# Kernel optimization log

Measured on AMD Instinct MI355X. Metric: run time of the kernel, lower is better.

Reference implementation:

```python
import jax, jax.numpy as jnp
import numpy as np

TREE_DEPTH = 3
CONSTANTS = jnp.array([-1.0, 0.0, 1.0], dtype=jnp.float32)


def setup_inputs() -> dict:
    key = jax.random.key(0)
    ks = jax.random.split(key, 5)
    B, S, D, W, SLOT = 2, 2048, 1024, 4096, 8
    C = SLOT + 3
    hidden = jax.random.normal(ks[0], (B, S, D), dtype=jnp.float32)
    slot_w = jax.random.normal(ks[1], (D, SLOT), dtype=jnp.float32) * (0.5 / np.sqrt(D))
    slot_b = jnp.zeros((SLOT,), dtype=jnp.float32)
    leaf_logits = jax.random.normal(ks[2], (W, 1 << TREE_DEPTH, C), dtype=jnp.float32) * 0.02
    node_params = jnp.array([1.0, 1.0, 0.25, 0.0, 0.0], dtype=jnp.float32)
    out_w = jax.random.normal(ks[3], (W, D), dtype=jnp.float32) * (0.5 / np.sqrt(W))
    out_b = jnp.zeros((D,), dtype=jnp.float32)
    return {"hidden": hidden, "slot_w": slot_w, "slot_b": slot_b,
            "leaf_logits": leaf_logits, "node_params": node_params,
            "out_w": out_w, "out_b": out_b}


def reference(hidden, slot_w, slot_b, leaf_logits, node_params, out_w, out_b):
    B, S, _ = hidden.shape
    # basis: tanh slot projection concatenated with fixed constants -> [B,S,slot+3]
    slots = jnp.tanh(hidden @ slot_w + slot_b)
    consts = jnp.broadcast_to(CONSTANTS.astype(hidden.dtype), (B, S, 3))
    basis = jnp.concatenate((slots, consts), axis=-1)
    # leaf values: softmax-weighted mixture over the tiny basis dim -> [B,S,W,leaf]
    selector = jax.nn.softmax(leaf_logits.astype(hidden.dtype), axis=-1)
    values = jnp.einsum('wlc,bsc->bswl', selector, basis)
    lw, rw, pw, dw, nb = [p.astype(hidden.dtype) for p in node_params]
    for _ in range(TREE_DEPTH):
        left, right = values[..., 0::2], values[..., 1::2]
        values = jnp.tanh(lw * left + rw * right + pw * left * right
                          + dw * (left - right) + nb)
    roots = values[..., 0]  # [B,S,W]
    return roots @ out_w + out_b
```

## Files before the change

kernel.cpp:

```cpp
#include <hip/hip_runtime.h>
#include <stdint.h>

#define BSZ   4096
#define DIM   1024
#define WTR   4096
#define KDIM  4096
#define W8    32768

typedef unsigned short u16;
typedef __attribute__((ext_vector_type(8))) short bhalf8;
typedef __attribute__((ext_vector_type(4))) float floatx4;
typedef __attribute__((ext_vector_type(16))) float floatx16;

__device__ __forceinline__ u16 f2bf(float f) {
    union { float f; uint32_t i; } v; v.f = f;
    uint32_t r = v.i + 0x7fffu + ((v.i >> 16) & 1u);
    return (u16)(r >> 16);
}
__device__ __forceinline__ float fast_tanh(float x) {
    float e = __builtin_amdgcn_exp2f(x * 2.885390081777927f);
    return fmaf(-2.0f, __builtin_amdgcn_rcpf(e + 1.0f), 1.0f);
}
__device__ __forceinline__ void load16(const void* g, void* lds) {
    __builtin_amdgcn_global_load_lds(
        (const __attribute__((address_space(1))) uint32_t*)g,
        (__attribute__((address_space(3))) uint32_t*)lds, 16, 0, 0);
}

__global__ __launch_bounds__(256) void k_prep(const float* __restrict__ ll,
                                              u16* __restrict__ selwA,
                                              const float* __restrict__ ow,
                                              u16* __restrict__ owt,
                                              const float* __restrict__ slot_w,
                                              u16* __restrict__ swT,
                                              const float* __restrict__ out_b,
                                              float* __restrict__ C) {
    int bid = blockIdx.x, tid = threadIdx.x;
    if (bid < 128) {
        int row = bid * 256 + tid;
        int w = row >> 3, l = row & 7, q = w & 3;
        int prow = (w >> 2) * 32 + (l & 3) + 8 * (l >> 2) + 16 * (q & 1) + 4 * (q >> 1);
        const float* p = ll + (size_t)row * 11;
        float v[11]; float m = -1e30f;
        #pragma unroll
        for (int c = 0; c < 11; ++c) { v[c] = p[c]; m = fmaxf(m, v[c]); }
        float s = 0.f;
        #pragma unroll
        for (int c = 0; c < 11; ++c) {
            v[c] = __builtin_amdgcn_exp2f((v[c] - m) * 1.4426950408889634f);
            s += v[c];
        }
        float inv = __builtin_amdgcn_rcpf(s);
        union { u16 h[16]; uint4 qq[2]; } o;
        #pragma unroll
        for (int c = 0; c < 8; ++c) o.h[c] = f2bf(v[c] * inv);
        o.h[8] = f2bf((v[10] - v[8]) * inv);
        #pragma unroll
        for (int c = 9; c < 16; ++c) o.h[c] = 0;
        uint4* dst = (uint4*)(selwA + (size_t)prow * 16);
        dst[0] = o.qq[0]; dst[1] = o.qq[1];
    } else if (bid < 128 + 4096) {
        int b = bid - 128;
        int d0 = (b & 31) * 32, w0 = (b >> 5) * 32;
        int tx = tid & 31, ty = tid >> 5;
        __shared__ float tile[32][33];
        #pragma unroll
        for (int i = 0; i < 32; i += 8)
            tile[ty + i][tx] = ow[(size_t)(w0 + ty + i) * DIM + d0 + tx];
        __syncthreads();
        #pragma unroll
        for (int i = 0; i < 32; i += 8)
            owt[(size_t)(d0 + ty + i) * WTR + w0 + tx] = f2bf(tile[tx][ty + i]);
    } else if (bid < 128 + 4096 + 8) {
        int b = bid - 128 - 4096;
        for (int it = 0; it < 8; ++it) {
            int idx = b * 2048 + it * 256 + tid;
            int s = idx >> 10, d = idx & 1023;
            float val = (s < 8) ? slot_w[(size_t)d * 8 + s] : 0.f;
            swT[(size_t)s * DIM + d] = f2bf(val);
        }
    } else {
        int b = bid - 128 - 4096 - 8;
        float4 bv = *(const float4*)(out_b + (tid & 255) * 4);
        #pragma unroll
        for (int it = 0; it < 16; ++it) {
            size_t flat = (size_t)b * 16384 + it * 1024 + (tid & 255) * 4;
            *(float4*)(C + flat) = bv;
        }
    }
}

__global__ __launch_bounds__(256) void k_basis(const float* __restrict__ hidden,
                                               const u16* __restrict__ swT,
                                               const float* __restrict__ slot_b,
                                               u16* __restrict__ basisTB) {
    int m0 = blockIdx.x * 16;
    int tid = threadIdx.x, lane = tid & 63, wid = tid >> 6;
    int col = lane & 15, quad = lane >> 4;
    const float* ga = hidden + (size_t)(m0 + col) * DIM + wid * 256 + quad * 8;
    const u16*   gb = swT + (size_t)col * DIM + wid * 256 + quad * 8;
    floatx4 acc = (floatx4){0.f, 0.f, 0.f, 0.f};
    #pragma unroll
    for (int k0 = 0; k0 < 256; k0 += 32) {
        float4 a0 = *(const float4*)(ga + k0);
        float4 a1 = *(const float4*)(ga + k0 + 4);
        bhalf8 bf = *(const bhalf8*)(gb + k0);
        bhalf8 af;
        af[0] = (short)f2bf(a0.x); af[1] = (short)f2bf(a0.y);
        af[2] = (short)f2bf(a0.z); af[3] = (short)f2bf(a0.w);
        af[4] = (short)f2bf(a1.x); af[5] = (short)f2bf(a1.y);
        af[6] = (short)f2bf(a1.z); af[7] = (short)f2bf(a1.w);
        acc = __builtin_amdgcn_mfma_f32_16x16x32_bf16(af, bf, acc, 0, 0, 0);
    }
    __shared__ float smr[4][16][16];
    #pragma unroll
    for (int r = 0; r < 4; ++r) smr[wid][quad * 4 + r][col] = acc[r];
    __syncthreads();
    int tt = tid >> 4, cc = tid & 15;
    float s = smr[0][tt][cc] + smr[1][tt][cc] + smr[2][tt][cc] + smr[3][tt][cc];
    u16 val;
    if (cc < 8)       val = f2bf(fast_tanh(s + slot_b[cc]));
    else if (cc == 8) val = (u16)0x3f80;
    else              val = 0;
    basisTB[(size_t)(m0 + tt) * 16 + cc] = val;
}

__device__ __forceinline__ float tree_eval(float v[8], float A1, float A2,
                                           float A3, float A4) {
    #pragma unroll
    for (int lev = 0; lev < 3; ++lev) {
        int n = 4 >> lev;
        #pragma unroll
        for (int i = 0; i < 4; ++i) {
            if (i < n) {
                float L = v[2*i], R = v[2*i+1];
                float u = fmaf(A2, R, A1);
                float w = fmaf(A3, R, A4);
                float y = fmaf(L, u, w);
                float e = __builtin_amdgcn_exp2f(y);
                v[i] = fmaf(-2.0f, __builtin_amdgcn_rcpf(e + 1.0f), 1.0f);
            }
        }
    }
    return v[0];
}

__global__ __launch_bounds__(256, 2) void k_roots(const u16* __restrict__ selwA,
                                                  const u16* __restrict__ basisTB,
                                                  const float* __restrict__ np_,
                                                  u16* __restrict__ roots) {
    __shared__ uint32_t st[2][32 * 33];
    int tid = threadIdx.x, wid = tid >> 6, lane = tid & 63;
    int c = lane & 31, h = lane >> 5;
    int tile0 = blockIdx.x * 16 + wid * 4;
    int wblk  = blockIdx.x * 64;
    int t0b   = blockIdx.y * 512;
    float lw = np_[0], rw = np_[1], pw = np_[2], dw = np_[3], nb = np_[4];
    const float c2 = 2.885390081777927f;
    float A1 = (lw + dw) * c2, A2 = pw * c2, A3 = (rw - dw) * c2, A4 = nb * c2;

    bhalf8 af[4];
    #pragma unroll
    for (int tl = 0; tl < 4; ++tl)
        af[tl] = *(const bhalf8*)(selwA + (size_t)((tile0 + tl) * 32 + c) * 16 + h * 8);

    int tok = tid >> 3, ch = tid & 7;
    for (int it = 0; it < 16; ++it) {
        int t0 = t0b + it * 32;
        uint32_t* buf = st[it & 1];
        bhalf8 bf = *(const bhalf8*)(basisTB + (size_t)(t0 + c) * 16 + h * 8);
        #pragma unroll
        for (int tl = 0; tl < 4; ++tl) {
            floatx16 z = {0.f,0.f,0.f,0.f,0.f,0.f,0.f,0.f,
                          0.f,0.f,0.f,0.f,0.f,0.f,0.f,0.f};
            floatx16 cc = __builtin_amdgcn_mfma_f32_32x32x16_bf16(af[tl], bf, z, 0, 0, 0);
            float vA[8], vB[8];
            #pragma unroll
            for (int l = 0; l < 8; ++l) { vA[l] = cc[l]; vB[l] = cc[8 + l]; }
            float rA = tree_eval(vA, A1, A2, A3, A4);
            float rB = tree_eval(vB, A1, A2, A3, A4);
            buf[c * 33 + wid * 8 + tl * 2 + h] =
                (uint32_t)f2bf(rA) | ((uint32_t)f2bf(rB) << 16);
        }
        __syncthreads();
        uint32_t d0 = buf[tok * 33 + ch * 4];
        uint32_t d1 = buf[tok * 33 + ch * 4 + 1];
        uint32_t d2 = buf[tok * 33 + ch * 4 + 2];
        uint32_t d3 = buf[tok * 33 + ch * 4 + 3];
        uint4 q; q.x = d0; q.y = d1; q.z = d2; q.w = d3;
        *(uint4*)(roots + (size_t)(t0 + tok) * WTR + wblk + ch * 8) = q;
    }
}

__global__ __launch_bounds__(256) void k_gemm(const u16* __restrict__ A,
                                              const u16* __restrict__ Bt,
                                              float* __restrict__ C) {
    __shared__ __align__(16) u16 smA[128 * 64];
    __shared__ __align__(16) u16 smB[128 * 64];
    int tid = threadIdx.x;
    int bm = blockIdx.x * 128, bn = blockIdx.y * 128;
    int koff = blockIdx.z * (KDIM / 2);
    int lane = tid & 63, wid = tid >> 6;
    int wm = (wid >> 1) * 64, wn = (wid & 1) * 64;

    floatx4 acc[4][4];
    #pragma unroll
    for (int i = 0; i < 4; ++i)
        #pragma unroll
        for (int j = 0; j < 4; ++j) acc[i][j] = (floatx4){0.f, 0.f, 0.f, 0.f};

    int ar = tid >> 3;
    int ak = ((tid & 7) ^ (ar & 7)) * 8;
    const u16* gA = A  + (size_t)(bm + ar) * KDIM + koff + ak;
    const u16* gB = Bt + (size_t)(bn + ar) * KDIM + koff + ak;
    char* ldA = (char*)smA + tid * 16;
    char* ldB = (char*)smB + tid * 16;

    int col = lane & 15, quad = lane >> 4, csw = col & 7;

    for (int k0 = 0; k0 < KDIM / 2 / 64; ++k0) {
        __syncthreads();
        load16(gA,                       ldA);
        load16(gA + (size_t)32 * KDIM,   ldA + 4096);
        load16(gA + (size_t)64 * KDIM,   ldA + 8192);
        load16(gA + (size_t)96 * KDIM,   ldA + 12288);
        load16(gB,                       ldB);
        load16(gB + (size_t)32 * KDIM,   ldB + 4096);
        load16(gB + (size_t)64 * KDIM,   ldB + 8192);
        load16(gB + (size_t)96 * KDIM,   ldB + 12288);
        gA += 64; gB += 64;
        __syncthreads();

        #pragma unroll
        for (int kk = 0; kk < 2; ++kk) {
            int kc = kk * 4 + quad;
            bhalf8 af[4], bf[4];
            #pragma unroll
            for (int i = 0; i < 4; ++i)
                af[i] = *(const bhalf8*)(smA + ((wm + i * 16 + col) * 8 + (kc ^ csw)) * 8);
            #pragma unroll
            for (int j = 0; j < 4; ++j)
                bf[j] = *(const bhalf8*)(smB + ((wn + j * 16 + col) * 8 + (kc ^ csw)) * 8);
            #pragma unroll
            for (int i = 0; i < 4; ++i)
                #pragma unroll
                for (int j = 0; j < 4; ++j)
                    acc[i][j] = __builtin_amdgcn_mfma_f32_16x16x32_bf16(
                        af[i], bf[j], acc[i][j], 0, 0, 0);
        }
    }

    #pragma unroll
    for (int j = 0; j < 4; ++j) {
        int n = bn + wn + j * 16 + col;
        #pragma unroll
        for (int i = 0; i < 4; ++i) {
            int m0 = bm + wm + i * 16 + quad * 4;
            #pragma unroll
            for (int r = 0; r < 4; ++r)
                atomicAdd(&C[(size_t)(m0 + r) * DIM + n], acc[i][j][r]);
        }
    }
}

extern "C" void kernel_launch(void* const* d_in, const int* in_sizes, int n_in,
                              void* d_out, int out_size, void* d_ws, size_t ws_size,
                              hipStream_t stream) {
    const float* hidden      = (const float*)d_in[0];
    const float* slot_w      = (const float*)d_in[1];
    const float* slot_b      = (const float*)d_in[2];
    const float* leaf_logits = (const float*)d_in[3];
    const float* node_params = (const float*)d_in[4];
    const float* out_w       = (const float*)d_in[5];
    const float* out_b       = (const float*)d_in[6];
    float* out = (float*)d_out;

    char* ws = (char*)d_ws;
    u16* selwA   = (u16*)ws;
    u16* basisTB = (u16*)(ws + 1048576);
    u16* swT     = (u16*)(ws + 1179648);
    u16* outwt   = (u16*)(ws + 1212416);
    u16* roots   = (u16*)(ws + 9601024);

    k_prep <<<128 + 4096 + 8 + 256, 256, 0, stream>>>(leaf_logits, selwA, out_w, outwt,
                                                      slot_w, swT, out_b, out);
    k_basis<<<BSZ / 16, 256, 0, stream>>>(hidden, swT, slot_b, basisTB);
    k_roots<<<dim3(64, 8), 256, 0, stream>>>(selwA, basisTB, node_params, roots);
    k_gemm <<<dim3(BSZ / 128, DIM / 128, 2), 256, 0, stream>>>(roots, outwt, out);
}
```

Measured before the change: 190.8 us.

## Fold basis projection into prep kernel and split GEMM K four ways

The separate basis-projection kernel is merged into the prep kernel as extra blocks. Each of those blocks transposes slot_w into shared memory itself, so the swT workspace buffer and one kernel launch go away. The output GEMM now splits K four ways instead of two, with a 32-wide K tile and smaller LDS tiles, which doubles the block count and the atomic adds into C. The prep kernel also grows its static shared memory to about 20KB for every block, which can lower occupancy for the transpose blocks.

Result: slower. 230.2 us (+20.7%).

```diff
diff --git a/kernel.cpp b/kernel.cpp
--- a/kernel.cpp
+++ b/kernel.cpp
@@ -27,16 +27,24 @@
         (__attribute__((address_space(3))) uint32_t*)lds, 16, 0, 0);
 }
 
+#define NB_SEL   128
+#define NB_OWT   4096
+#define NB_CINIT 256
+#define NB_BASIS 256
+
 __global__ __launch_bounds__(256) void k_prep(const float* __restrict__ ll,
                                               u16* __restrict__ selwA,
                                               const float* __restrict__ ow,
                                               u16* __restrict__ owt,
                                               const float* __restrict__ slot_w,
-                                              u16* __restrict__ swT,
+                                              const float* __restrict__ slot_b,
                                               const float* __restrict__ out_b,
-                                              float* __restrict__ C) {
+                                              float* __restrict__ C,
+                                              const float* __restrict__ hidden,
+                                              u16* __restrict__ basisTB) {
+    __shared__ __align__(16) char smem[20608];
     int bid = blockIdx.x, tid = threadIdx.x;
-    if (bid < 128) {
+    if (bid < NB_SEL) {
         int row = bid * 256 + tid;
         int w = row >> 3, l = row & 7, q = w & 3;
         int prow = (w >> 2) * 32 + (l & 3) + 8 * (l >> 2) + 16 * (q & 1) + 4 * (q >> 1);
@@ -59,11 +67,11 @@
         for (int c = 9; c < 16; ++c) o.h[c] = 0;
         uint4* dst = (uint4*)(selwA + (size_t)prow * 16);
         dst[0] = o.qq[0]; dst[1] = o.qq[1];
-    } else if (bid < 128 + 4096) {
-        int b = bid - 128;
+    } else if (bid < NB_SEL + NB_OWT) {
+        float (*tile)[33] = (float (*)[33])smem;
+        int b = bid - NB_SEL;
         int d0 = (b & 31) * 32, w0 = (b >> 5) * 32;
         int tx = tid & 31, ty = tid >> 5;
-        __shared__ float tile[32][33];
         #pragma unroll
         for (int i = 0; i < 32; i += 8)
             tile[ty + i][tx] = ow[(size_t)(w0 + ty + i) * DIM + d0 + tx];
@@ -71,58 +79,55 @@
         #pragma unroll
         for (int i = 0; i < 32; i += 8)
             owt[(size_t)(d0 + ty + i) * WTR + w0 + tx] = f2bf(tile[tx][ty + i]);
-    } else if (bid < 128 + 4096 + 8) {
-        int b = bid - 128 - 4096;
-        for (int it = 0; it < 8; ++it) {
-            int idx = b * 2048 + it * 256 + tid;
-            int s = idx >> 10, d = idx & 1023;
-            float val = (s < 8) ? slot_w[(size_t)d * 8 + s] : 0.f;
-            swT[(size_t)s * DIM + d] = f2bf(val);
+    } else if (bid < NB_SEL + NB_OWT + NB_CINIT) {
+        int b = bid - NB_SEL - NB_OWT;
+        float4 bv = *(const float4*)(out_b + tid * 4);
+        #pragma unroll
+        for (int it = 0; it < 16; ++it) {
+            size_t flat = (size_t)b * 16384 + it * 1024 + tid * 4;
+            *(float4*)(C + flat) = bv;
         }
     } else {
-        int b = bid - 128 - 4096 - 8;
-        float4 bv = *(const float4*)(out_b + (tid & 255) * 4);
-        #pragma unroll
-        for (int it = 0; it < 16; ++it) {
-            size_t flat = (size_t)b * 16384 + it * 1024 + (tid & 255) * 4;
-            *(float4*)(C + flat) = bv;
-        }
-    }
-}
-
-__global__ __launch_bounds__(256) void k_basis(const float* __restrict__ hidden,
-                                               const u16* __restrict__ swT,
-                                               const float* __restrict__ slot_b,
-                                               u16* __restrict__ basisTB) {
-    int m0 = blockIdx.x * 16;
-    int tid = threadIdx.x, lane = tid & 63, wid = tid >> 6;
-    int col = lane & 15, quad = lane >> 4;
-    const float* ga = hidden + (size_t)(m0 + col) * DIM + wid * 256 + quad * 8;
-    const u16*   gb = swT + (size_t)col * DIM + wid * 256 + quad * 8;
-    floatx4 acc = (floatx4){0.f, 0.f, 0.f, 0.f};
-    #pragma unroll
-    for (int k0 = 0; k0 < 256; k0 += 32) {
-        float4 a0 = *(const float4*)(ga + k0);
-        float4 a1 = *(const float4*)(ga + k0 + 4);
-        bhalf8 bf = *(const bhalf8*)(gb + k0);
-        bhalf8 af;
-        af[0] = (short)f2bf(a0.x); af[1] = (short)f2bf(a0.y);
-        af[2] = (short)f2bf(a0.z); af[3] = (short)f2bf(a0.w);
-        af[4] = (short)f2bf(a1.x); af[5] = (short)f2bf(a1.y);
-        af[6] = (short)f2bf(a1.z); af[7] = (short)f2bf(a1.w);
-        acc = __builtin_amdgcn_mfma_f32_16x16x32_bf16(af, bf, acc, 0, 0, 0);
-    }
-    __shared__ float smr[4][16][16];
-    #pragma unroll
-    for (int r = 0; r < 4; ++r) smr[wid][quad * 4 + r][col] = acc[r];
-    __syncthreads();
-    int tt = tid >> 4, cc = tid & 15;
-    float s = smr[0][tt][cc] + smr[1][tt][cc] + smr[2][tt][cc] + smr[3][tt][cc];
-    u16 val;
-    if (cc < 8)       val = f2bf(fast_tanh(s + slot_b[cc]));
-    else if (cc == 8) val = (u16)0x3f80;
-    else              val = 0;
-    basisTB[(size_t)(m0 + tt) * 16 + cc] = val;
+        u16*   sw  = (u16*)smem;
+        float* smr = (float*)(smem + 16384);
+        int b = bid - NB_SEL - NB_OWT - NB_CINIT;
+        int m0 = b * 16;
+        for (int i = tid; i < 8 * 1024; i += 256) {
+            int d = i & 1023, s = i >> 10;
+            sw[s * 1024 + d] = f2bf(slot_w[(size_t)d * 8 + s]);
+        }
+        __syncthreads();
+        int lane = tid & 63, wid = tid >> 6;
+        int col = lane & 15, quad = lane >> 4;
+        const float* ga = hidden + (size_t)(m0 + col) * DIM + wid * 256 + quad * 8;
+        const u16*   gb = sw + (col & 7) * 1024 + wid * 256 + quad * 8;
+        bhalf8 zz = {0, 0, 0, 0, 0, 0, 0, 0};
+        floatx4 acc = (floatx4){0.f, 0.f, 0.f, 0.f};
+        #pragma unroll
+        for (int k0 = 0; k0 < 256; k0 += 32) {
+            float4 a0 = *(const float4*)(ga + k0);
+            float4 a1 = *(const float4*)(ga + k0 + 4);
+            bhalf8 bf = *(const bhalf8*)(gb + k0);
+            if (col >= 8) bf = zz;
+            bhalf8 af;
+            af[0] = (short)f2bf(a0.x); af[1] = (short)f2bf(a0.y);
+            af[2] = (short)f2bf(a0.z); af[3] = (short)f2bf(a0.w);
+            af[4] = (short)f2bf(a1.x); af[5] = (short)f2bf(a1.y);
+            af[6] = (short)f2bf(a1.z); af[7] = (short)f2bf(a1.w);
+            acc = __builtin_amdgcn_mfma_f32_16x16x32_bf16(af, bf, acc, 0, 0, 0);
+        }
+        float (*sm3)[16][16] = (float (*)[16][16])smr;
+        #pragma unroll
+        for (int r = 0; r < 4; ++r) sm3[wid][quad * 4 + r][col] = acc[r];
+        __syncthreads();
+        int tt = tid >> 4, cc = tid & 15;
+        float s = sm3[0][tt][cc] + sm3[1][tt][cc] + sm3[2][tt][cc] + sm3[3][tt][cc];
+        u16 val;
+        if (cc < 8)       val = f2bf(fast_tanh(s + slot_b[cc]));
+        else if (cc == 8) val = (u16)0x3f80;
+        else              val = 0;
+        basisTB[(size_t)(m0 + tt) * 16 + cc] = val;
+    }
 }
 
 __device__ __forceinline__ float tree_eval(float v[8], float A1, float A2,
@@ -195,11 +200,11 @@
 __global__ __launch_bounds__(256) void k_gemm(const u16* __restrict__ A,
                                               const u16* __restrict__ Bt,
                                               float* __restrict__ C) {
-    __shared__ __align__(16) u16 smA[128 * 64];
-    __shared__ __align__(16) u16 smB[128 * 64];
+    __shared__ __align__(16) u16 smA[128 * 32];
+    __shared__ __align__(16) u16 smB[128 * 32];
     int tid = threadIdx.x;
     int bm = blockIdx.x * 128, bn = blockIdx.y * 128;
-    int koff = blockIdx.z * (KDIM / 2);
+    int koff = blockIdx.z * (KDIM / 4);
     int lane = tid & 63, wid = tid >> 6;
     int wm = (wid >> 1) * 64, wn = (wid & 1) * 64;
 
@@ -209,45 +214,38 @@
         #pragma unroll
         for (int j = 0; j < 4; ++j) acc[i][j] = (floatx4){0.f, 0.f, 0.f, 0.f};
 
-    int ar = tid >> 3;
-    int ak = ((tid & 7) ^ (ar & 7)) * 8;
+    int ar = tid >> 2;
+    int ak = ((tid & 3) ^ (ar & 3)) * 8;
     const u16* gA = A  + (size_t)(bm + ar) * KDIM + koff + ak;
     const u16* gB = Bt + (size_t)(bn + ar) * KDIM + koff + ak;
     char* ldA = (char*)smA + tid * 16;
     char* ldB = (char*)smB + tid * 16;
 
-    int col = lane & 15, quad = lane >> 4, csw = col & 7;
-
-    for (int k0 = 0; k0 < KDIM / 2 / 64; ++k0) {
+    int col = lane & 15, quad = lane >> 4, csw = col & 3;
+
+    for (int k0 = 0; k0 < KDIM / 4; k0 += 32) {
         __syncthreads();
         load16(gA,                       ldA);
-        load16(gA + (size_t)32 * KDIM,   ldA + 4096);
-        load16(gA + (size_t)64 * KDIM,   ldA + 8192);
-        load16(gA + (size_t)96 * KDIM,   ldA + 12288);
+        load16(gA + (size_t)64 * KDIM,   ldA + 4096);
         load16(gB,                       ldB);
-        load16(gB + (size_t)32 * KDIM,   ldB + 4096);
-        load16(gB + (size_t)64 * KDIM,   ldB + 8192);
-        load16(gB + (size_t)96 * KDIM,   ldB + 12288);
-        gA += 64; gB += 64;
-        __syncthreads();
-
-        #pragma unroll
-        for (int kk = 0; kk < 2; ++kk) {
-            int kc = kk * 4 + quad;
-            bhalf8 af[4], bf[4];
-            #pragma unroll
-            for (int i = 0; i < 4; ++i)
-                af[i] = *(const bhalf8*)(smA + ((wm + i * 16 + col) * 8 + (kc ^ csw)) * 8);
+        load16(gB + (size_t)64 * KDIM,   ldB + 4096);
+        gA += 32; gB += 32;
+        __syncthreads();
+
+        bhalf8 af[4], bf[4];
+        int kchunk = (quad ^ csw) * 8;
+        #pragma unroll
+        for (int i = 0; i < 4; ++i)
+            af[i] = *(const bhalf8*)(smA + (wm + i * 16 + col) * 32 + kchunk);
+        #pragma unroll
+        for (int j = 0; j < 4; ++j)
+            bf[j] = *(const bhalf8*)(smB + (wn + j * 16 + col) * 32 + kchunk);
+        #pragma unroll
+        for (int i = 0; i < 4; ++i)
             #pragma unroll
             for (int j = 0; j < 4; ++j)
-                bf[j] = *(const bhalf8*)(smB + ((wn + j * 16 + col) * 8 + (kc ^ csw)) * 8);
-            #pragma unroll
-            for (int i = 0; i < 4; ++i)
-                #pragma unroll
-                for (int j = 0; j < 4; ++j)
-                    acc[i][j] = __builtin_amdgcn_mfma_f32_16x16x32_bf16(
-                        af[i], bf[j], acc[i][j], 0, 0, 0);
-        }
+                acc[i][j] = __builtin_amdgcn_mfma_f32_16x16x32_bf16(
+                    af[i], bf[j], acc[i][j], 0, 0, 0);
     }
 
     #pragma unroll
@@ -278,13 +276,11 @@
     char* ws = (char*)d_ws;
     u16* selwA   = (u16*)ws;
     u16* basisTB = (u16*)(ws + 1048576);
-    u16* swT     = (u16*)(ws + 1179648);
     u16* outwt   = (u16*)(ws + 1212416);
     u16* roots   = (u16*)(ws + 9601024);
 
-    k_prep <<<128 + 4096 + 8 + 256, 256, 0, stream>>>(leaf_logits, selwA, out_w, outwt,
-                                                      slot_w, swT, out_b, out);
-    k_basis<<<BSZ / 16, 256, 0, stream>>>(hidden, swT, slot_b, basisTB);
+    k_prep <<<NB_SEL + NB_OWT + NB_CINIT + NB_BASIS, 256, 0, stream>>>(
+        leaf_logits, selwA, out_w, outwt, slot_w, slot_b, out_b, out, hidden, basisTB);
     k_roots<<<dim3(64, 8), 256, 0, stream>>>(selwA, basisTB, node_params, roots);
-    k_gemm <<<dim3(BSZ / 128, DIM / 128, 2), 256, 0, stream>>>(roots, outwt, out);
-}
+    k_gemm <<<dim3(BSZ / 128, DIM / 128, 4), 256, 0, stream>>>(roots, outwt, out);
+}
```
